# Kernel optimization log

Measured on AMD Instinct MI355X. Metric: run time of the kernel, lower is better.

The kernel has to match this reference:

```python
import jax, jax.numpy as jnp
import numpy as np

B = 1048576  # batch
H = 64       # rnn_hid_units


def _lstm_final(x, Wih, Whh, bih, bhh):
    """Single-layer LSTM over x: [T, B, 1]; returns final (h, c), each [B, H].
    PyTorch gate order: i, f, g, o."""
    Bn = x.shape[1]
    Hd = Whh.shape[1]
    b = bih + bhh  # fuse both bias vectors
    h0 = jnp.zeros((Bn, Hd), x.dtype)
    c0 = jnp.zeros((Bn, Hd), x.dtype)

    def step(carry, xt):
        h, c = carry
        gates = xt @ Wih.T + h @ Whh.T + b  # [B, 4H]
        i, f, g, o = jnp.split(gates, 4, axis=-1)
        i = jax.nn.sigmoid(i)
        f = jax.nn.sigmoid(f)
        g = jnp.tanh(g)
        o = jax.nn.sigmoid(o)
        c = f * c + i * g
        h = o * jnp.tanh(c)
        return (h, c), None

    (h, c), _ = jax.lax.scan(step, (h0, c0), x)
    return h, c


def setup_inputs() -> dict:
    key = jax.random.key(0)
    ks = jax.random.split(key, 18)

    def rn(k, shape, s=0.1):
        return jax.random.normal(k, shape, dtype=jnp.float32) * s

    inp = {
        "inputs": jax.random.normal(ks[0], (B, 18), dtype=jnp.float32),
        # encoder1 (nn.LSTM(1, H), single layer)
        "Wih1": rn(ks[1], (4 * H, 1)),
        "Whh1": rn(ks[2], (4 * H, H)),
        "bih1": rn(ks[3], (4 * H,)),
        "bhh1": rn(ks[4], (4 * H,)),
        # encoder2
        "Wih2": rn(ks[5], (4 * H, 1)),
        "Whh2": rn(ks[6], (4 * H, H)),
        "bih2": rn(ks[7], (4 * H,)),
        "bhh2": rn(ks[8], (4 * H,)),
        # MLP feat_trans: 2 -> 64 -> 64 -> 32 (ReLU between, linear output)
        "mW0": rn(ks[9], (64, 2)),
        "mb0": rn(ks[10], (64,)),
        "mW1": rn(ks[11], (64, 64)),
        "mb1": rn(ks[12], (64,)),
        "mW2": rn(ks[13], (32, 64)),
        "mb2": rn(ks[14], (32,)),
        # projector: 4H + 32 = 288 -> 2
        "pW": rn(ks[15], (2, 4 * H + 32)),
        "pb": rn(ks[16], (2,)),
    }
    return inp


def reference(inputs, Wih1, Whh1, bih1, bhh1, Wih2, Whh2, bih2, bhh2,
              mW0, mb0, mW1, mb1, mW2, mb2, pW, pb):
    # split_with_sizes([8, 8, 2], dim=-1)
    seq1 = inputs[:, :8].T[:, :, None]    # [8, B, 1]
    seq2 = inputs[:, 8:16].T[:, :, None]  # [8, B, 1]
    feat = inputs[:, 16:]                 # [B, 2]

    h1, c1 = _lstm_final(seq1, Wih1, Whh1, bih1, bhh1)  # [B, H] each
    h2, c2 = _lstm_final(seq2, Wih2, Whh2, bih2, bhh2)

    hid = jax.nn.relu(feat @ mW0.T + mb0)
    hid = jax.nn.relu(hid @ mW1.T + mb1)
    hid = hid @ mW2.T + mb2  # [B, 32]

    z = jnp.concatenate([h1, c1, h2, c2, hid], axis=-1)  # [B, 4H+32]
    return z @ pW.T + pb
```

## Files before the change

### kernel.cpp

```cpp
#include <hip/hip_runtime.h>

#define BLOCK 256
#define HROW 72

typedef _Float16 half_t;
typedef __attribute__((ext_vector_type(8))) _Float16 half8;
typedef __attribute__((ext_vector_type(4))) float float4v;

#define L2E  1.4426950408889634f
#define L2E2 2.8853900817779268f

__device__ __forceinline__ float rcp_(float x) { return __builtin_amdgcn_rcpf(x); }
__device__ __forceinline__ float ex2(float x)  { return __builtin_amdgcn_exp2f(x); }

extern "C" __global__ void __launch_bounds__(BLOCK, 1) mlp_kernel(
    const float* __restrict__ inputs,
    const float* __restrict__ mW0, const float* __restrict__ mb0,
    const float* __restrict__ mW1, const float* __restrict__ mb1,
    const float* __restrict__ mW2, const float* __restrict__ mb2,
    const float* __restrict__ pW, const float* __restrict__ pb,
    float* __restrict__ out, int n)
{
    int b = blockIdx.x * BLOCK + threadIdx.x;
    if (b >= n) return;
    float f0 = inputs[(size_t)b * 18 + 16], f1 = inputs[(size_t)b * 18 + 17];
    float h0[64];
    #pragma unroll
    for (int i = 0; i < 64; ++i)
        h0[i] = fmaxf(fmaf(mW0[2 * i], f0, fmaf(mW0[2 * i + 1], f1, mb0[i])), 0.0f);
    float acc2[32];
    #pragma unroll
    for (int j = 0; j < 32; ++j) acc2[j] = mb2[j];
    #pragma unroll 2
    for (int i = 0; i < 64; ++i) {
        float a = mb1[i];
        #pragma unroll
        for (int k = 0; k < 64; ++k) a = fmaf(mW1[i * 64 + k], h0[k], a);
        a = fmaxf(a, 0.0f);
        #pragma unroll
        for (int j = 0; j < 32; ++j) acc2[j] = fmaf(mW2[j * 64 + i], a, acc2[j]);
    }
    float out0 = pb[0], out1 = pb[1];
    #pragma unroll
    for (int j = 0; j < 32; ++j) {
        out0 = fmaf(pW[256 + j], acc2[j], out0);
        out1 = fmaf(pW[288 + 256 + j], acc2[j], out1);
    }
    ((float2*)out)[b] = make_float2(out0, out1);
}

template <bool LAST>
__device__ __forceinline__ void lstm_step(
    const float* __restrict__ xt,
    const half_t* __restrict__ src, half_t* __restrict__ dst,
    const half8 Bf[4][2], const float wih_v[4], const float bias_v[4],
    int l15, int quad, int jcol,
    float4v cst[4],
    const float* __restrict__ pWz,
    float* __restrict__ wpw)
{
    float ph0, pc0, ph1, pc1;
    if (LAST) {
        ph0 = pWz[jcol];       pc0 = pWz[64 + jcol];
        ph1 = pWz[288 + jcol]; pc1 = pWz[288 + 64 + jcol];
    }
    #pragma unroll
    for (int mt = 0; mt < 4; ++mt) {
        float4v x4 = *(const float4v*)&xt[mt * 16 + quad * 4];
        half8 a0 = *(const half8*)&src[(mt * 16 + l15) * HROW + quad * 8];
        half8 a1 = *(const half8*)&src[(mt * 16 + l15) * HROW + 32 + quad * 8];
        float4v ag[4];
        #pragma unroll
        for (int gg = 0; gg < 4; ++gg) {
            float4v ai;
            #pragma unroll
            for (int reg = 0; reg < 4; ++reg) ai[reg] = fmaf(x4[reg], wih_v[gg], bias_v[gg]);
            ai = __builtin_amdgcn_mfma_f32_16x16x32_f16(a0, Bf[gg][0], ai, 0, 0, 0);
            ai = __builtin_amdgcn_mfma_f32_16x16x32_f16(a1, Bf[gg][1], ai, 0, 0, 0);
            ag[gg] = ai;
        }
        float po0[4], po1[4];
        #pragma unroll
        for (int reg = 0; reg < 4; ++reg) {
            float Bi  = ex2(ag[0][reg]);
            float Bff = ex2(ag[1][reg]);
            float Bg  = ex2(ag[2][reg]);
            float Bo  = ex2(ag[3][reg]);
            float P   = (1.0f + Bi) * (1.0f + Bg);
            float F   = 1.0f + Bff;
            float t2  = fmaf(Bi, Bg, -Bi);
            float t1  = Bff * cst[mt][reg] * P;
            float num = fmaf(t2, F, t1);
            float cn  = num * rcp_(P * F);
            cst[mt][reg] = cn;
            float Cc  = ex2(cn * L2E2);
            float hv  = fmaf(Bo, Cc, -Bo) * rcp_((1.0f + Bo) * (1.0f + Cc));
            if (LAST) {
                po0[reg] = fmaf(ph0, hv, pc0 * cn);
                po1[reg] = fmaf(ph1, hv, pc1 * cn);
            } else {
                dst[(mt * 16 + quad * 4 + reg) * HROW + jcol] = (half_t)hv;
            }
        }
        if (LAST) {
            #pragma unroll
            for (int reg = 0; reg < 4; ++reg) {
                #pragma unroll
                for (int s = 1; s < 16; s <<= 1) {
                    po0[reg] += __shfl_xor(po0[reg], s, 64);
                    po1[reg] += __shfl_xor(po1[reg], s, 64);
                }
            }
            if (l15 == 0) {
                #pragma unroll
                for (int reg = 0; reg < 4; ++reg) {
                    int m = mt * 16 + quad * 4 + reg;
                    wpw[m * 2]     += po0[reg];
                    wpw[m * 2 + 1] += po1[reg];
                }
            }
        }
    }
    __syncthreads();
}

__device__ __forceinline__ void lstm_mfma_one(
    const float* __restrict__ Wih, const float* __restrict__ Whh,
    const float* __restrict__ bih, const float* __restrict__ bhh,
    const float* __restrict__ pW, int zbase,
    const float* __restrict__ xt,
    half_t* __restrict__ hbuf,
    int w, int lane,
    float* __restrict__ wpw)
{
    const int l15  = lane & 15;
    const int quad = lane >> 4;
    const int jcol = w * 16 + l15;

    const float gscale[4] = {L2E, L2E, L2E2, L2E};
    half8 Bf[4][2];
    float wih_v[4], bias_v[4];
    #pragma unroll
    for (int gg = 0; gg < 4; ++gg) {
        const int nrow = gg * 64 + jcol;
        const float s = gscale[gg];
        #pragma unroll
        for (int kf = 0; kf < 2; ++kf) {
            const float4* p = (const float4*)(Whh + nrow * 64 + kf * 32 + quad * 8);
            float4 w0 = p[0], w1 = p[1];
            Bf[gg][kf] = half8{(half_t)(w0.x * s), (half_t)(w0.y * s), (half_t)(w0.z * s), (half_t)(w0.w * s),
                               (half_t)(w1.x * s), (half_t)(w1.y * s), (half_t)(w1.z * s), (half_t)(w1.w * s)};
        }
        wih_v[gg]  = Wih[nrow] * s;
        bias_v[gg] = (bih[nrow] + bhh[nrow]) * s;
    }

    float4v cst[4];

    #pragma unroll
    for (int mt = 0; mt < 4; ++mt) {
        float4v x4 = *(const float4v*)&xt[mt * 16 + quad * 4];
        #pragma unroll
        for (int reg = 0; reg < 4; ++reg) {
            float Bi = ex2(fmaf(x4[reg], wih_v[0], bias_v[0]));
            float Bg = ex2(fmaf(x4[reg], wih_v[2], bias_v[2]));
            float Bo = ex2(fmaf(x4[reg], wih_v[3], bias_v[3]));
            float cn = fmaf(Bi, Bg, -Bi) * rcp_((1.0f + Bi) * (1.0f + Bg));
            cst[mt][reg] = cn;
            float Cc = ex2(cn * L2E2);
            float hv = fmaf(Bo, Cc, -Bo) * rcp_((1.0f + Bo) * (1.0f + Cc));
            hbuf[(mt * 16 + quad * 4 + reg) * HROW + jcol] = (half_t)hv;
        }
    }
    __syncthreads();

    half_t* b0 = hbuf;
    half_t* b1 = hbuf + 64 * HROW;
    #pragma unroll 1
    for (int tt = 1; tt < 7; tt += 2) {
        lstm_step<false>(xt + tt * 64,       b0, b1, Bf, wih_v, bias_v, l15, quad, jcol,
                         cst, pW, wpw);
        lstm_step<false>(xt + (tt + 1) * 64, b1, b0, Bf, wih_v, bias_v, l15, quad, jcol,
                         cst, pW, wpw);
    }
    lstm_step<true>(xt + 7 * 64, b0, b1, Bf, wih_v, bias_v, l15, quad, jcol,
                    cst, pW + zbase, wpw);
}

extern "C" __global__ void __launch_bounds__(BLOCK, 3) lstm_mfma(
    const float* __restrict__ inputs,
    const float* __restrict__ Wih1, const float* __restrict__ Whh1,
    const float* __restrict__ bih1, const float* __restrict__ bhh1,
    const float* __restrict__ Wih2, const float* __restrict__ Whh2,
    const float* __restrict__ bih2, const float* __restrict__ bhh2,
    const float* __restrict__ pW,
    float* __restrict__ out, int n)
{
    __shared__ half_t hbuf[2 * 64 * HROW];
    __shared__ float  xt_lds[16 * 64];
    __shared__ float  wp[4][64][2];

    const int tid  = threadIdx.x;
    const int w    = tid >> 6;
    const int lane = tid & 63;
    const int base = blockIdx.x * 64;

    ((float2*)wp)[tid] = make_float2(0.0f, 0.0f);
    for (int idx = tid; idx < 64 * 18; idx += BLOCK) {
        int row = idx / 18, c = idx % 18;
        float v = inputs[(size_t)(base + row) * 18 + c];
        if (c < 16) xt_lds[c * 64 + row] = v;
    }
    __syncthreads();

    float* wpw = &wp[w][0][0];
    lstm_mfma_one(Wih1, Whh1, bih1, bhh1, pW, 0,   xt_lds,          hbuf, w, lane, wpw);
    lstm_mfma_one(Wih2, Whh2, bih2, bhh2, pW, 128, xt_lds + 8 * 64, hbuf, w, lane, wpw);

    if (tid < 64) {
        int gb = base + tid;
        float2 o = ((float2*)out)[gb];
        o.x += wp[0][tid][0] + wp[1][tid][0] + wp[2][tid][0] + wp[3][tid][0];
        o.y += wp[0][tid][1] + wp[1][tid][1] + wp[2][tid][1] + wp[3][tid][1];
        ((float2*)out)[gb] = o;
    }
}

extern "C" void kernel_launch(void* const* d_in, const int* in_sizes, int n_in,
                              void* d_out, int out_size, void* d_ws, size_t ws_size,
                              hipStream_t stream) {
    const int n = in_sizes[0] / 18;
    mlp_kernel<<<(n + BLOCK - 1) / BLOCK, BLOCK, 0, stream>>>(
        (const float*)d_in[0],
        (const float*)d_in[9],  (const float*)d_in[10],
        (const float*)d_in[11], (const float*)d_in[12],
        (const float*)d_in[13], (const float*)d_in[14],
        (const float*)d_in[15], (const float*)d_in[16],
        (float*)d_out, n);
    lstm_mfma<<<n / 64, BLOCK, 0, stream>>>(
        (const float*)d_in[0],
        (const float*)d_in[1], (const float*)d_in[2],
        (const float*)d_in[3], (const float*)d_in[4],
        (const float*)d_in[5], (const float*)d_in[6],
        (const float*)d_in[7], (const float*)d_in[8],
        (const float*)d_in[15],
        (float*)d_out, n);
}
```

Measured before the change: 1.788 ms.

## Restructure LSTM kernel with per-wave 32-row batches, 32x32 MFMA and LDS-staged Whh

Each wave now owns 32 batch rows and computes all 64 hidden units for them with 32x32x16 MFMAs. Whh is staged in shared memory as scaled fp16 and read as the B operand each step, replacing the old register-resident fragments. The hidden state stays in a per-wave LDS buffer, so the per-timestep __syncthreads goes away and each block covers 128 rows instead of 64. The cost is more LDS traffic for weights, larger per-thread accumulators, and occupancy lowered to 2 blocks per CU.

```diff
diff --git a/kernel.cpp b/kernel.cpp
--- a/kernel.cpp
+++ b/kernel.cpp
@@ -1,11 +1,12 @@
 #include <hip/hip_runtime.h>
 
 #define BLOCK 256
-#define HROW 72
+#define WHH_STRIDE 76
 
 typedef _Float16 half_t;
-typedef __attribute__((ext_vector_type(8))) _Float16 half8;
-typedef __attribute__((ext_vector_type(4))) float float4v;
+typedef __attribute__((ext_vector_type(4)))  _Float16 half4;
+typedef __attribute__((ext_vector_type(8)))  _Float16 half8;
+typedef __attribute__((ext_vector_type(16))) float   float16v;
 
 #define L2E  1.4426950408889634f
 #define L2E2 2.8853900817779268f
@@ -49,145 +50,170 @@
     ((float2*)out)[b] = make_float2(out0, out1);
 }
 
+
+__device__ __forceinline__ void stage_whh(const float* __restrict__ Whh,
+                                          half_t* __restrict__ whh_lds, int tid)
+{
+    #pragma unroll
+    for (int it = 0; it < 16; ++it) {
+        int idx4 = tid + it * 256;
+        int row  = idx4 >> 4;
+        int c4   = idx4 & 15;
+        float4 v = ((const float4*)Whh)[idx4];
+        float  s = ((row >> 6) == 2) ? L2E2 : L2E;
+        half4  h = {(half_t)(v.x * s), (half_t)(v.y * s), (half_t)(v.z * s), (half_t)(v.w * s)};
+        *(half4*)&whh_lds[row * WHH_STRIDE + c4 * 4] = h;
+    }
+}
+
 template <bool LAST>
 __device__ __forceinline__ void lstm_step(
     const float* __restrict__ xt,
-    const half_t* __restrict__ src, half_t* __restrict__ dst,
-    const half8 Bf[4][2], const float wih_v[4], const float bias_v[4],
-    int l15, int quad, int jcol,
-    float4v cst[4],
-    const float* __restrict__ pWz,
-    float* __restrict__ wpw)
-{
-    float ph0, pc0, ph1, pc1;
+    const half_t* __restrict__ whh_lds,
+    half_t* __restrict__ hw,
+    const float wih_s[4][2], const float bias_s[4][2],
+    const float ph0[2], const float pc0[2], const float ph1[2], const float pc1[2],
+    int w, int l31, int hi,
+    float cst[2][16],
+    float* __restrict__ wp)
+{
+    half8 A[4];
+    #pragma unroll
+    for (int kf = 0; kf < 4; ++kf)
+        A[kf] = *(const half8*)&hw[l31 * WHH_STRIDE + kf * 16 + hi * 8];
+    float4 x4[4];
+    #pragma unroll
+    for (int rq = 0; rq < 4; ++rq)
+        x4[rq] = *(const float4*)&xt[w * 32 + rq * 8 + hi * 4];
+
+    float po0[16], po1[16];
     if (LAST) {
-        ph0 = pWz[jcol];       pc0 = pWz[64 + jcol];
-        ph1 = pWz[288 + jcol]; pc1 = pWz[288 + 64 + jcol];
-    }
-    #pragma unroll
-    for (int mt = 0; mt < 4; ++mt) {
-        float4v x4 = *(const float4v*)&xt[mt * 16 + quad * 4];
-        half8 a0 = *(const half8*)&src[(mt * 16 + l15) * HROW + quad * 8];
-        half8 a1 = *(const half8*)&src[(mt * 16 + l15) * HROW + 32 + quad * 8];
-        float4v ag[4];
-        #pragma unroll
-        for (int gg = 0; gg < 4; ++gg) {
-            float4v ai;
-            #pragma unroll
-            for (int reg = 0; reg < 4; ++reg) ai[reg] = fmaf(x4[reg], wih_v[gg], bias_v[gg]);
-            ai = __builtin_amdgcn_mfma_f32_16x16x32_f16(a0, Bf[gg][0], ai, 0, 0, 0);
-            ai = __builtin_amdgcn_mfma_f32_16x16x32_f16(a1, Bf[gg][1], ai, 0, 0, 0);
-            ag[gg] = ai;
-        }
-        float po0[4], po1[4];
-        #pragma unroll
-        for (int reg = 0; reg < 4; ++reg) {
-            float Bi  = ex2(ag[0][reg]);
-            float Bff = ex2(ag[1][reg]);
-            float Bg  = ex2(ag[2][reg]);
-            float Bo  = ex2(ag[3][reg]);
+        #pragma unroll
+        for (int r = 0; r < 16; ++r) { po0[r] = 0.0f; po1[r] = 0.0f; }
+    }
+
+    #pragma unroll
+    for (int jt = 0; jt < 2; ++jt) {
+        float16v acc[4];
+        #pragma unroll
+        for (int g = 0; g < 4; ++g) {
+            float16v a;
+            #pragma unroll
+            for (int reg = 0; reg < 16; ++reg)
+                a[reg] = fmaf(((const float*)&x4[reg >> 2])[reg & 3], wih_s[g][jt], bias_s[g][jt]);
+            #pragma unroll
+            for (int kf = 0; kf < 4; ++kf) {
+                half8 B = *(const half8*)&whh_lds[(g * 64 + jt * 32 + l31) * WHH_STRIDE + kf * 16 + hi * 8];
+                a = __builtin_amdgcn_mfma_f32_32x32x16_f16(A[kf], B, a, 0, 0, 0);
+            }
+            acc[g] = a;
+        }
+        #pragma unroll
+        for (int reg = 0; reg < 16; ++reg) {
+            float Bi  = ex2(acc[0][reg]);
+            float Bff = ex2(acc[1][reg]);
+            float Bg  = ex2(acc[2][reg]);
+            float Bo  = ex2(acc[3][reg]);
             float P   = (1.0f + Bi) * (1.0f + Bg);
             float F   = 1.0f + Bff;
             float t2  = fmaf(Bi, Bg, -Bi);
-            float t1  = Bff * cst[mt][reg] * P;
-            float num = fmaf(t2, F, t1);
-            float cn  = num * rcp_(P * F);
-            cst[mt][reg] = cn;
+            float t1  = Bff * cst[jt][reg] * P;
+            float cn  = fmaf(t2, F, t1) * rcp_(P * F);
+            cst[jt][reg] = cn;
             float Cc  = ex2(cn * L2E2);
             float hv  = fmaf(Bo, Cc, -Bo) * rcp_((1.0f + Bo) * (1.0f + Cc));
             if (LAST) {
-                po0[reg] = fmaf(ph0, hv, pc0 * cn);
-                po1[reg] = fmaf(ph1, hv, pc1 * cn);
+                po0[reg] = fmaf(ph0[jt], hv, fmaf(pc0[jt], cn, po0[reg]));
+                po1[reg] = fmaf(ph1[jt], hv, fmaf(pc1[jt], cn, po1[reg]));
             } else {
-                dst[(mt * 16 + quad * 4 + reg) * HROW + jcol] = (half_t)hv;
-            }
-        }
-        if (LAST) {
-            #pragma unroll
-            for (int reg = 0; reg < 4; ++reg) {
-                #pragma unroll
-                for (int s = 1; s < 16; s <<= 1) {
-                    po0[reg] += __shfl_xor(po0[reg], s, 64);
-                    po1[reg] += __shfl_xor(po1[reg], s, 64);
-                }
-            }
-            if (l15 == 0) {
-                #pragma unroll
-                for (int reg = 0; reg < 4; ++reg) {
-                    int m = mt * 16 + quad * 4 + reg;
-                    wpw[m * 2]     += po0[reg];
-                    wpw[m * 2 + 1] += po1[reg];
-                }
-            }
-        }
-    }
-    __syncthreads();
-}
-
-__device__ __forceinline__ void lstm_mfma_one(
-    const float* __restrict__ Wih, const float* __restrict__ Whh,
-    const float* __restrict__ bih, const float* __restrict__ bhh,
+                int m = (reg & 3) + 8 * (reg >> 2) + 4 * hi;
+                hw[m * WHH_STRIDE + jt * 32 + l31] = (half_t)hv;
+            }
+        }
+    }
+
+    if (LAST) {
+        #pragma unroll
+        for (int reg = 0; reg < 16; ++reg) {
+            #pragma unroll
+            for (int s = 1; s < 32; s <<= 1) {
+                po0[reg] += __shfl_xor(po0[reg], s, 64);
+                po1[reg] += __shfl_xor(po1[reg], s, 64);
+            }
+        }
+        if (l31 == 0) {
+            #pragma unroll
+            for (int reg = 0; reg < 16; ++reg) {
+                int m = w * 32 + (reg & 3) + 8 * (reg >> 2) + 4 * hi;
+                wp[m * 2]     += po0[reg];
+                wp[m * 2 + 1] += po1[reg];
+            }
+        }
+    }
+}
+
+__device__ __forceinline__ void lstm_run(
+    const float* __restrict__ Wih, const float* __restrict__ bih, const float* __restrict__ bhh,
     const float* __restrict__ pW, int zbase,
-    const float* __restrict__ xt,
-    half_t* __restrict__ hbuf,
-    int w, int lane,
-    float* __restrict__ wpw)
-{
-    const int l15  = lane & 15;
-    const int quad = lane >> 4;
-    const int jcol = w * 16 + l15;
-
-    const float gscale[4] = {L2E, L2E, L2E2, L2E};
-    half8 Bf[4][2];
-    float wih_v[4], bias_v[4];
-    #pragma unroll
-    for (int gg = 0; gg < 4; ++gg) {
-        const int nrow = gg * 64 + jcol;
-        const float s = gscale[gg];
-        #pragma unroll
-        for (int kf = 0; kf < 2; ++kf) {
-            const float4* p = (const float4*)(Whh + nrow * 64 + kf * 32 + quad * 8);
-            float4 w0 = p[0], w1 = p[1];
-            Bf[gg][kf] = half8{(half_t)(w0.x * s), (half_t)(w0.y * s), (half_t)(w0.z * s), (half_t)(w0.w * s),
-                               (half_t)(w1.x * s), (half_t)(w1.y * s), (half_t)(w1.z * s), (half_t)(w1.w * s)};
-        }
-        wih_v[gg]  = Wih[nrow] * s;
-        bias_v[gg] = (bih[nrow] + bhh[nrow]) * s;
-    }
-
-    float4v cst[4];
-
-    #pragma unroll
-    for (int mt = 0; mt < 4; ++mt) {
-        float4v x4 = *(const float4v*)&xt[mt * 16 + quad * 4];
-        #pragma unroll
-        for (int reg = 0; reg < 4; ++reg) {
-            float Bi = ex2(fmaf(x4[reg], wih_v[0], bias_v[0]));
-            float Bg = ex2(fmaf(x4[reg], wih_v[2], bias_v[2]));
-            float Bo = ex2(fmaf(x4[reg], wih_v[3], bias_v[3]));
-            float cn = fmaf(Bi, Bg, -Bi) * rcp_((1.0f + Bi) * (1.0f + Bg));
-            cst[mt][reg] = cn;
-            float Cc = ex2(cn * L2E2);
-            float hv = fmaf(Bo, Cc, -Bo) * rcp_((1.0f + Bo) * (1.0f + Cc));
-            hbuf[(mt * 16 + quad * 4 + reg) * HROW + jcol] = (half_t)hv;
-        }
-    }
-    __syncthreads();
-
-    half_t* b0 = hbuf;
-    half_t* b1 = hbuf + 64 * HROW;
+    const half_t* __restrict__ whh_lds, const float* __restrict__ xt,
+    half_t* __restrict__ hw, int w, int lane, float* __restrict__ wp)
+{
+    const int l31 = lane & 31;
+    const int hi  = lane >> 5;
+
+    float wih_s[4][2], bias_s[4][2];
+    #pragma unroll
+    for (int g = 0; g < 4; ++g) {
+        float s = (g == 2) ? L2E2 : L2E;
+        #pragma unroll
+        for (int jt = 0; jt < 2; ++jt) {
+            int nn = g * 64 + jt * 32 + l31;
+            wih_s[g][jt]  = Wih[nn] * s;
+            bias_s[g][jt] = (bih[nn] + bhh[nn]) * s;
+        }
+    }
+    float ph0[2], pc0[2], ph1[2], pc1[2];
+    #pragma unroll
+    for (int jt = 0; jt < 2; ++jt) {
+        int j = jt * 32 + l31;
+        ph0[jt] = pW[zbase + j];       pc0[jt] = pW[zbase + 64 + j];
+        ph1[jt] = pW[288 + zbase + j]; pc1[jt] = pW[288 + zbase + 64 + j];
+    }
+
+    float cst[2][16];
+
+    {
+        float4 x4[4];
+        #pragma unroll
+        for (int rq = 0; rq < 4; ++rq)
+            x4[rq] = *(const float4*)&xt[w * 32 + rq * 8 + hi * 4];
+        #pragma unroll
+        for (int jt = 0; jt < 2; ++jt) {
+            #pragma unroll
+            for (int reg = 0; reg < 16; ++reg) {
+                float xv = ((const float*)&x4[reg >> 2])[reg & 3];
+                float Bi = ex2(fmaf(xv, wih_s[0][jt], bias_s[0][jt]));
+                float Bg = ex2(fmaf(xv, wih_s[2][jt], bias_s[2][jt]));
+                float Bo = ex2(fmaf(xv, wih_s[3][jt], bias_s[3][jt]));
+                float cn = fmaf(Bi, Bg, -Bi) * rcp_((1.0f + Bi) * (1.0f + Bg));
+                cst[jt][reg] = cn;
+                float Cc = ex2(cn * L2E2);
+                float hv = fmaf(Bo, Cc, -Bo) * rcp_((1.0f + Bo) * (1.0f + Cc));
+                int m = (reg & 3) + 8 * (reg >> 2) + 4 * hi;
+                hw[m * WHH_STRIDE + jt * 32 + l31] = (half_t)hv;
+            }
+        }
+    }
+
     #pragma unroll 1
-    for (int tt = 1; tt < 7; tt += 2) {
-        lstm_step<false>(xt + tt * 64,       b0, b1, Bf, wih_v, bias_v, l15, quad, jcol,
-                         cst, pW, wpw);
-        lstm_step<false>(xt + (tt + 1) * 64, b1, b0, Bf, wih_v, bias_v, l15, quad, jcol,
-                         cst, pW, wpw);
-    }
-    lstm_step<true>(xt + 7 * 64, b0, b1, Bf, wih_v, bias_v, l15, quad, jcol,
-                    cst, pW + zbase, wpw);
-}
-
-extern "C" __global__ void __launch_bounds__(BLOCK, 3) lstm_mfma(
+    for (int t = 1; t < 7; ++t)
+        lstm_step<false>(xt + t * 128, whh_lds, hw, wih_s, bias_s,
+                         ph0, pc0, ph1, pc1, w, l31, hi, cst, wp);
+    lstm_step<true>(xt + 7 * 128, whh_lds, hw, wih_s, bias_s,
+                    ph0, pc0, ph1, pc1, w, l31, hi, cst, wp);
+}
+
+extern "C" __global__ void __launch_bounds__(BLOCK, 2) lstm_mfma(
     const float* __restrict__ inputs,
     const float* __restrict__ Wih1, const float* __restrict__ Whh1,
     const float* __restrict__ bih1, const float* __restrict__ bhh1,
@@ -196,32 +222,40 @@
     const float* __restrict__ pW,
     float* __restrict__ out, int n)
 {
-    __shared__ half_t hbuf[2 * 64 * HROW];
-    __shared__ float  xt_lds[16 * 64];
-    __shared__ float  wp[4][64][2];
+    __shared__ half_t whh_lds[256 * WHH_STRIDE];
+    __shared__ half_t hbuf[4][32 * WHH_STRIDE];
+    __shared__ float  xt_lds[16 * 128];
+    __shared__ float  wp[128][2];
 
     const int tid  = threadIdx.x;
     const int w    = tid >> 6;
     const int lane = tid & 63;
-    const int base = blockIdx.x * 64;
-
-    ((float2*)wp)[tid] = make_float2(0.0f, 0.0f);
-    for (int idx = tid; idx < 64 * 18; idx += BLOCK) {
+    const int base = blockIdx.x * 128;
+
+    wp[tid >> 1][tid & 1] = 0.0f;
+    stage_whh(Whh1, whh_lds, tid);
+    for (int idx = tid; idx < 128 * 18; idx += BLOCK) {
         int row = idx / 18, c = idx % 18;
         float v = inputs[(size_t)(base + row) * 18 + c];
-        if (c < 16) xt_lds[c * 64 + row] = v;
-    }
-    __syncthreads();
-
-    float* wpw = &wp[w][0][0];
-    lstm_mfma_one(Wih1, Whh1, bih1, bhh1, pW, 0,   xt_lds,          hbuf, w, lane, wpw);
-    lstm_mfma_one(Wih2, Whh2, bih2, bhh2, pW, 128, xt_lds + 8 * 64, hbuf, w, lane, wpw);
-
-    if (tid < 64) {
+        if (c < 16) xt_lds[c * 128 + row] = v;
+    }
+    __syncthreads();
+
+    half_t* hw = &hbuf[w][0];
+    lstm_run(Wih1, bih1, bhh1, pW, 0, whh_lds, xt_lds, hw, w, lane, &wp[0][0]);
+
+    __syncthreads();
+    stage_whh(Whh2, whh_lds, tid);
+    __syncthreads();
+
+    lstm_run(Wih2, bih2, bhh2, pW, 128, whh_lds, xt_lds + 8 * 128, hw, w, lane, &wp[0][0]);
+
+    __syncthreads();
+    if (tid < 128) {
         int gb = base + tid;
         float2 o = ((float2*)out)[gb];
-        o.x += wp[0][tid][0] + wp[1][tid][0] + wp[2][tid][0] + wp[3][tid][0];
-        o.y += wp[0][tid][1] + wp[1][tid][1] + wp[2][tid][1] + wp[3][tid][1];
+        o.x += wp[tid][0];
+        o.y += wp[tid][1];
         ((float2*)out)[gb] = o;
     }
 }
@@ -237,7 +271,7 @@
         (const float*)d_in[13], (const float*)d_in[14],
         (const float*)d_in[15], (const float*)d_in[16],
         (float*)d_out, n);
-    lstm_mfma<<<n / 64, BLOCK, 0, stream>>>(
+    lstm_mfma<<<n / 128, BLOCK, 0, stream>>>(
         (const float*)d_in[0],
         (const float*)d_in[1], (const float*)d_in[2],
         (const float*)d_in[3], (const float*)d_in[4],
```

New measurement: 6.988 ms. +290.8%, slower.
